# Performance work log

Hardware: AMD Instinct MI355X
Metric: run time of the kernel (lower is better)

## Reference

```python
import jax, jax.numpy as jnp
import numpy as np

K_HALF = 512
BUCKETS = 8
FV_SCALE = 16
SHIFT = 6
FT_SHIFT = 0
FT_IN = 32 * 704 + 704  # FT_IN_DIMS + VIRTUAL = 23232
B = 4096


def setup_inputs() -> dict:
    key = jax.random.key(0)
    ks = jax.random.split(key, 11)
    s = 0.02
    return {
        "bucket": jax.random.randint(ks[0], (B, 1), 0, BUCKETS, dtype=jnp.int64 if jax.config.jax_enable_x64 else jnp.int32).astype(jnp.int32),
        "features1": jax.random.uniform(ks[1], (B, FT_IN), dtype=jnp.float32),
        "features2": jax.random.uniform(ks[2], (B, FT_IN), dtype=jnp.float32),
        "ft_w": s * jax.random.normal(ks[3], (K_HALF + BUCKETS, FT_IN), dtype=jnp.float32),
        "ft_b": s * jax.random.normal(ks[4], (K_HALF + BUCKETS,), dtype=jnp.float32),
        "h1_w": s * jax.random.normal(ks[5], (16 * BUCKETS, 2 * K_HALF), dtype=jnp.float32),
        "h1_b": s * jax.random.normal(ks[6], (16 * BUCKETS,), dtype=jnp.float32),
        "h2_w": s * jax.random.normal(ks[7], (32 * BUCKETS, 16), dtype=jnp.float32),
        "h2_b": s * jax.random.normal(ks[8], (32 * BUCKETS,), dtype=jnp.float32),
        "out_w": s * jax.random.normal(ks[9], (BUCKETS, 32), dtype=jnp.float32),
        "out_b": jnp.zeros((BUCKETS,), dtype=jnp.float32),
    }


def reference(bucket, features1, features2, ft_w, ft_b, h1_w, h1_b, h2_w, h2_b, out_w, out_b):
    clamp = lambda x: jnp.clip(x, 0.0, 1.0)
    a1 = features1 @ ft_w.T + ft_b  # [B, 520]
    a2 = features2 @ ft_w.T + ft_b
    f1, psqt1 = a1[:, :K_HALF], a1[:, K_HALF:]
    f2, psqt2 = a2[:, :K_HALF], a2[:, K_HALF:]
    psqt = 0.5 * (jnp.take_along_axis(psqt1, bucket, axis=1)
                  - jnp.take_along_axis(psqt2, bucket, axis=1))  # [B,1]
    ft_out = clamp(jnp.concatenate([f1, f2], axis=1))  # [B, 1024]
    h1 = (ft_out @ h1_w.T + h1_b).reshape(-1, BUCKETS, 16)
    h1 = clamp(jnp.take_along_axis(h1, bucket[:, :, None], axis=1)[:, 0])  # [B,16]
    h2 = (h1 @ h2_w.T + h2_b).reshape(-1, BUCKETS, 32)
    h2 = clamp(jnp.take_along_axis(h2, bucket[:, :, None], axis=1)[:, 0])  # [B,32]
    out = h2 @ out_w.T + out_b  # [B, 8]
    return jnp.take_along_axis(out, bucket, axis=1) + (FV_SCALE * 2 ** FT_SHIFT) * psqt / 2 ** SHIFT
```

## Files before the change

kernel.cpp:

```cpp
#include <hip/hip_runtime.h>
#include <hip/hip_bf16.h>
#include <stdint.h>

typedef __attribute__((ext_vector_type(8))) short short8v;
typedef __attribute__((ext_vector_type(4))) short short4v;
typedef __attribute__((ext_vector_type(4))) float floatx4;

#define K_DIM   23232
#define BATCH   4096
#define M_TOT   8192
#define BM      128
#define BMG     256
#define BN      176
#define BK      64
#define N_PAD   528
#define N_REAL  520

__device__ __forceinline__ float clamp01(float x) {
    return fminf(fmaxf(x, 0.0f), 1.0f);
}

__device__ __forceinline__ short8v cvt8(float4 a, float4 b) {
    union { short8v s; __hip_bfloat16 h[8]; } u;
    u.h[0] = __float2bfloat16(a.x); u.h[1] = __float2bfloat16(a.y);
    u.h[2] = __float2bfloat16(a.z); u.h[3] = __float2bfloat16(a.w);
    u.h[4] = __float2bfloat16(b.x); u.h[5] = __float2bfloat16(b.y);
    u.h[6] = __float2bfloat16(b.z); u.h[7] = __float2bfloat16(b.w);
    return u.s;
}

#define GLOAD_LDS16(g, l) __builtin_amdgcn_global_load_lds(               \
    (const __attribute__((address_space(1))) void*)(g),                   \
    (__attribute__((address_space(3))) void*)(l), 16, 0, 0)

__global__ __launch_bounds__(256) void convert_bf16(
    const float* __restrict__ f1, const float* __restrict__ f2,
    const float* __restrict__ ftw,
    __hip_bfloat16* __restrict__ A, __hip_bfloat16* __restrict__ B)
{
    const size_t totalA = (size_t)M_TOT * K_DIM;
    const size_t halfA  = totalA / 2;
    const size_t totalB = (size_t)N_PAD * K_DIM;
    const size_t realB  = (size_t)N_REAL * K_DIM;
    size_t idx    = ((size_t)blockIdx.x * blockDim.x + threadIdx.x) * 8;
    size_t stride = (size_t)gridDim.x * blockDim.x * 8;

    for (size_t i = idx; i < totalA; i += stride) {
        const float* src = (i < halfA) ? (f1 + i) : (f2 + (i - halfA));
        float4 v0 = *(const float4*)(src);
        float4 v1 = *(const float4*)(src + 4);
        *(short8v*)(A + i) = cvt8(v0, v1);
    }
    for (size_t i = idx; i < totalB; i += stride) {
        if (i < realB) {
            float4 v0 = *(const float4*)(ftw + i);
            float4 v1 = *(const float4*)(ftw + i + 4);
            *(short8v*)(B + i) = cvt8(v0, v1);
        } else {
            *(short8v*)(B + i) = (short8v){0,0,0,0,0,0,0,0};
        }
    }
}

__global__ __launch_bounds__(256, 2) void ft_gemm(
    const __hip_bfloat16* __restrict__ A,
    const __hip_bfloat16* __restrict__ B,
    float* __restrict__ part, int kiters)
{
    __shared__ __align__(16) __hip_bfloat16 As[BMG][BK];
    __shared__ __align__(16) __hip_bfloat16 Bs[BN][BK];

    const int t    = threadIdx.x;
    const int w    = t >> 6;
    const int lane = t & 63;
    const int quad = lane >> 4;
    const int l16  = lane & 15;
    const int r7   = l16 & 7;

    const int cpx = gridDim.x >> 3;
    const int h   = blockIdx.x;
    const int lid = (h & 7) * cpx + (h >> 3);
    const int xb  = lid % 3;
    const int rst = lid / 3;
    const int yb  = rst & 31;
    const int zb  = rst >> 5;

    const int n0 = xb * BN;
    const int m0 = yb * BMG;
    int k0 = zb * kiters * BK;
    const int kEnd = k0 + kiters * BK;

    const int arow = lane >> 3;
    const int acol = ((lane & 7) ^ (lane >> 3)) * 8;

    floatx4 acc[4][11];
#pragma unroll
    for (int i = 0; i < 4; ++i)
#pragma unroll
        for (int j = 0; j < 11; ++j)
            acc[i][j] = (floatx4){0.f, 0.f, 0.f, 0.f};

    for (; k0 < kEnd; k0 += BK) {
        __syncthreads();
#pragma unroll
        for (int i = 0; i < 8; ++i) {
            int R = w * 8 + i * 32;
            const __hip_bfloat16* g =
                A + (size_t)(m0 + R + arow) * K_DIM + k0 + acol;
            GLOAD_LDS16(g, &As[R][0]);
        }
        for (int R = w * 8; R < BN; R += 32) {
            const __hip_bfloat16* g =
                B + (size_t)(n0 + R + arow) * K_DIM + k0 + acol;
            GLOAD_LDS16(g, &Bs[R][0]);
        }
        __syncthreads();
#pragma unroll
        for (int ks = 0; ks < BK; ks += 32) {
            const int slot = ((ks >> 3) + quad) ^ r7;
            short8v a[4];
#pragma unroll
            for (int mi = 0; mi < 4; ++mi)
                a[mi] = *(const short8v*)(&As[w * 64 + mi * 16 + l16][slot * 8]);
#pragma unroll
            for (int nf = 0; nf < 11; ++nf) {
                short8v b = *(const short8v*)(&Bs[nf * 16 + l16][slot * 8]);
#pragma unroll
                for (int mi = 0; mi < 4; ++mi)
                    acc[mi][nf] = __builtin_amdgcn_mfma_f32_16x16x32_bf16(
                        a[mi], b, acc[mi][nf], 0, 0, 0);
            }
        }
    }

    float* __restrict__ dst = part + (size_t)zb * ((size_t)M_TOT * N_PAD);
#pragma unroll
    for (int mi = 0; mi < 4; ++mi) {
#pragma unroll
        for (int nf = 0; nf < 11; ++nf) {
            int gn = n0 + nf * 16 + l16;
#pragma unroll
            for (int r = 0; r < 4; ++r) {
                int gm = m0 + w * 64 + mi * 16 + quad * 4 + r;
                dst[(size_t)gm * N_PAD + gn] = acc[mi][nf][r];
            }
        }
    }
}

__global__ __launch_bounds__(256) void ft_gemm_fused(
    const float* __restrict__ f1, const float* __restrict__ f2,
    const float* __restrict__ ftw, float* __restrict__ part, int kiters)
{
    __shared__ __align__(16) __hip_bfloat16 As[BM][72];
    __shared__ __align__(16) __hip_bfloat16 Bs[BN][72];

    const int t    = threadIdx.x;
    const int w    = t >> 6;
    const int lane = t & 63;
    const int quad = lane >> 4;
    const int l16  = lane & 15;

    const int n0 = blockIdx.x * BN;
    const int m0 = blockIdx.y * BM;
    const int z  = blockIdx.z;
    int k0 = z * kiters * BK;
    const int kEnd = k0 + kiters * BK;

    const float* __restrict__ srcA =
        (m0 < BATCH) ? (f1 + (size_t)m0 * K_DIM)
                     : (f2 + (size_t)(m0 - BATCH) * K_DIM);

    floatx4 acc[2][11];
#pragma unroll
    for (int i = 0; i < 2; ++i)
#pragma unroll
        for (int j = 0; j < 11; ++j)
            acc[i][j] = (floatx4){0.f, 0.f, 0.f, 0.f};

    for (; k0 < kEnd; k0 += BK) {
        __syncthreads();
#pragma unroll
        for (int it = 0; it < 8; ++it) {
            int c = t + it * 256, row = c >> 4, col = (c & 15) * 4;
            float4 v = *(const float4*)(srcA + (size_t)row * K_DIM + k0 + col);
            union { short4v s; __hip_bfloat16 h[4]; } u;
            u.h[0] = __float2bfloat16(v.x); u.h[1] = __float2bfloat16(v.y);
            u.h[2] = __float2bfloat16(v.z); u.h[3] = __float2bfloat16(v.w);
            *(short4v*)(&As[row][col]) = u.s;
        }
#pragma unroll
        for (int it = 0; it < 11; ++it) {
            int c = t + it * 256, row = c >> 4, col = (c & 15) * 4;
            int gn = n0 + row;
            float4 v = (gn < N_REAL)
                ? *(const float4*)(ftw + (size_t)gn * K_DIM + k0 + col)
                : make_float4(0.f, 0.f, 0.f, 0.f);
            union { short4v s; __hip_bfloat16 h[4]; } u;
            u.h[0] = __float2bfloat16(v.x); u.h[1] = __float2bfloat16(v.y);
            u.h[2] = __float2bfloat16(v.z); u.h[3] = __float2bfloat16(v.w);
            *(short4v*)(&Bs[row][col]) = u.s;
        }
        __syncthreads();
#pragma unroll
        for (int ks = 0; ks < BK; ks += 32) {
            short8v a0 = *(const short8v*)(&As[w * 32 + l16][ks + quad * 8]);
            short8v a1 = *(const short8v*)(&As[w * 32 + 16 + l16][ks + quad * 8]);
#pragma unroll
            for (int nf = 0; nf < 11; ++nf) {
                short8v b = *(const short8v*)(&Bs[nf * 16 + l16][ks + quad * 8]);
                acc[0][nf] = __builtin_amdgcn_mfma_f32_16x16x32_bf16(a0, b, acc[0][nf], 0, 0, 0);
                acc[1][nf] = __builtin_amdgcn_mfma_f32_16x16x32_bf16(a1, b, acc[1][nf], 0, 0, 0);
            }
        }
    }

    float* __restrict__ dst = part + (size_t)z * ((size_t)M_TOT * N_PAD);
#pragma unroll
    for (int mi = 0; mi < 2; ++mi) {
#pragma unroll
        for (int nf = 0; nf < 11; ++nf) {
            int gn = n0 + nf * 16 + l16;
#pragma unroll
            for (int r = 0; r < 4; ++r) {
                int gm = m0 + w * 32 + mi * 16 + quad * 4 + r;
                dst[(size_t)gm * N_PAD + gn] = acc[mi][nf][r];
            }
        }
    }
}

__global__ __launch_bounds__(256) void nnue_tail(
    const float* __restrict__ part, int ksplit,
    const int*   __restrict__ bucket,
    const float* __restrict__ ft_b,
    const float* __restrict__ h1_w, const float* __restrict__ h1_b,
    const float* __restrict__ h2_w, const float* __restrict__ h2_b,
    const float* __restrict__ out_w, const float* __restrict__ out_b,
    float* __restrict__ out)
{
    const int m = blockIdx.x;
    const int b = bucket[m];
    const size_t sz = (size_t)M_TOT * N_PAD;

    __shared__ float ft[1024];
    __shared__ float h1s[16];

    const float* p1 = part + (size_t)m * N_PAD;
    const float* p2 = part + (size_t)(m + BATCH) * N_PAD;

    for (int i = threadIdx.x; i < 1024; i += 256) {
        const float* pr = (i < 512) ? p1 : p2;
        int ci = i & 511;
        float v = ft_b[ci];
        for (int s = 0; s < ksplit; ++s) v += pr[ci + s * sz];
        ft[i] = clamp01(v);
    }
    __syncthreads();

    const int w    = threadIdx.x >> 6;
    const int lane = threadIdx.x & 63;

#pragma unroll
    for (int i = 0; i < 4; ++i) {
        int row = b * 16 + w * 4 + i;
        const float* wr = h1_w + (size_t)row * 1024;
        float s = 0.f;
#pragma unroll
        for (int c = 0; c < 16; ++c)
            s += ft[c * 64 + lane] * wr[c * 64 + lane];
#pragma unroll
        for (int off = 32; off > 0; off >>= 1)
            s += __shfl_down(s, off);
        if (lane == 0) h1s[w * 4 + i] = clamp01(s + h1_b[row]);
    }
    __syncthreads();

    if (threadIdx.x < 32) {
        int i = threadIdx.x;
        const float* wr = h2_w + (size_t)(b * 32 + i) * 16;
        float s = h2_b[b * 32 + i];
#pragma unroll
        for (int j = 0; j < 16; ++j) s += wr[j] * h1s[j];
        float prod = clamp01(s) * out_w[b * 32 + i];
#pragma unroll
        for (int off = 16; off > 0; off >>= 1)
            prod += __shfl_down(prod, off);
        if (i == 0) {
            float v1 = 0.f, v2 = 0.f;
            for (int s2 = 0; s2 < ksplit; ++s2) {
                v1 += p1[512 + b + s2 * sz];
                v2 += p2[512 + b + s2 * sz];
            }
            out[m] = prod + out_b[b] + 0.125f * (v1 - v2);
        }
    }
}

extern "C" void kernel_launch(void* const* d_in, const int* in_sizes, int n_in,
                              void* d_out, int out_size, void* d_ws, size_t ws_size,
                              hipStream_t stream) {
    const int*   bucket = (const int*)  d_in[0];
    const float* f1     = (const float*)d_in[1];
    const float* f2     = (const float*)d_in[2];
    const float* ftw    = (const float*)d_in[3];
    const float* ftb    = (const float*)d_in[4];
    const float* h1w    = (const float*)d_in[5];
    const float* h1b    = (const float*)d_in[6];
    const float* h2w    = (const float*)d_in[7];
    const float* h2b    = (const float*)d_in[8];
    const float* outw   = (const float*)d_in[9];
    const float* outb   = (const float*)d_in[10];
    float* out = (float*)d_out;

    const size_t szA = (size_t)M_TOT * K_DIM * sizeof(__hip_bfloat16);
    const size_t szB = (size_t)N_PAD * K_DIM * sizeof(__hip_bfloat16);
    const size_t szPart1 = (size_t)M_TOT * N_PAD * sizeof(float);

    int ksplit;
    if (ws_size >= szA + szB + 11 * szPart1)      ksplit = 11;
    else if (ws_size >= szA + szB + 3 * szPart1)  ksplit = 3;
    else                                          ksplit = 0;

    if (ksplit > 0) {
        __hip_bfloat16* A = (__hip_bfloat16*)d_ws;
        __hip_bfloat16* Bm = (__hip_bfloat16*)((char*)d_ws + szA);
        float* part = (float*)((char*)d_ws + szA + szB);
        int kiters = 363 / ksplit;

        convert_bf16<<<4096, 256, 0, stream>>>(f1, f2, ftw, A, Bm);
        int nblk = 3 * 32 * ksplit;
        ft_gemm<<<dim3(nblk), 256, 0, stream>>>(A, Bm, part, kiters);
        nnue_tail<<<BATCH, 256, 0, stream>>>(part, ksplit, bucket, ftb,
                                             h1w, h1b, h2w, h2b, outw, outb, out);
    } else {
        float* part = (float*)d_ws;
        dim3 grid1(3, 64, 3);
        ft_gemm_fused<<<grid1, 256, 0, stream>>>(f1, f2, ftw, part, 121);
        nnue_tail<<<BATCH, 256, 0, stream>>>(part, 3, bucket, ftb,
                                             h1w, h1b, h2w, h2b, outw, outb, out);
    }
}
```

Baseline: 1.140 ms.

## Fuse fp32-to-bf16 activation conversion into GEMM A-tile loads

Removes the separate pass that converted both feature matrices to bf16 in workspace. The GEMM now loads fp32 activations directly, converts them in registers and writes them into a swizzled LDS layout, so the large round trip through an intermediate bf16 copy of A is gone. Only the weight matrix is still pre-converted. The tail kernel is also templated on the split count and uses vectorized float4 partial-sum reduction. The trade-off is that A tile loads now go through registers rather than direct global-to-LDS transfers, and each fp32 A element is read once per N tile (three times) at twice the bf16 size.

```diff
diff --git a/kernel.cpp b/kernel.cpp
--- a/kernel.cpp
+++ b/kernel.cpp
@@ -29,28 +29,25 @@
     return u.s;
 }
 
+__device__ __forceinline__ short4v cvt4(float4 a) {
+    union { short4v s; __hip_bfloat16 h[4]; } u;
+    u.h[0] = __float2bfloat16(a.x); u.h[1] = __float2bfloat16(a.y);
+    u.h[2] = __float2bfloat16(a.z); u.h[3] = __float2bfloat16(a.w);
+    return u.s;
+}
+
 #define GLOAD_LDS16(g, l) __builtin_amdgcn_global_load_lds(               \
     (const __attribute__((address_space(1))) void*)(g),                   \
     (__attribute__((address_space(3))) void*)(l), 16, 0, 0)
 
-__global__ __launch_bounds__(256) void convert_bf16(
-    const float* __restrict__ f1, const float* __restrict__ f2,
-    const float* __restrict__ ftw,
-    __hip_bfloat16* __restrict__ A, __hip_bfloat16* __restrict__ B)
+__global__ __launch_bounds__(256) void convert_B(
+    const float* __restrict__ ftw, __hip_bfloat16* __restrict__ B)
 {
-    const size_t totalA = (size_t)M_TOT * K_DIM;
-    const size_t halfA  = totalA / 2;
     const size_t totalB = (size_t)N_PAD * K_DIM;
     const size_t realB  = (size_t)N_REAL * K_DIM;
     size_t idx    = ((size_t)blockIdx.x * blockDim.x + threadIdx.x) * 8;
     size_t stride = (size_t)gridDim.x * blockDim.x * 8;
 
-    for (size_t i = idx; i < totalA; i += stride) {
-        const float* src = (i < halfA) ? (f1 + i) : (f2 + (i - halfA));
-        float4 v0 = *(const float4*)(src);
-        float4 v1 = *(const float4*)(src + 4);
-        *(short8v*)(A + i) = cvt8(v0, v1);
-    }
     for (size_t i = idx; i < totalB; i += stride) {
         if (i < realB) {
             float4 v0 = *(const float4*)(ftw + i);
@@ -62,8 +59,8 @@
     }
 }
 
-__global__ __launch_bounds__(256, 2) void ft_gemm(
-    const __hip_bfloat16* __restrict__ A,
+__global__ __launch_bounds__(256, 2) void ft_gemm_af32(
+    const float* __restrict__ f1, const float* __restrict__ f2,
     const __hip_bfloat16* __restrict__ B,
     float* __restrict__ part, int kiters)
 {
@@ -90,9 +87,19 @@
     int k0 = zb * kiters * BK;
     const int kEnd = k0 + kiters * BK;
 
+    const float* __restrict__ srcA =
+        (m0 < BATCH) ? (f1 + (size_t)m0 * K_DIM)
+                     : (f2 + (size_t)(m0 - BATCH) * K_DIM);
+
     const int arow = lane >> 3;
     const int acol = ((lane & 7) ^ (lane >> 3)) * 8;
 
+    const int tr  = t >> 4;
+    const int c4  = t & 15;
+    const int ps  = (c4 >> 1) ^ (tr & 7);
+    char* const aLds = (char*)&As[0][0] + tr * 128 + ps * 16 + (c4 & 1) * 8;
+    const float* const aG = srcA + (size_t)tr * K_DIM + c4 * 4;
+
     floatx4 acc[4][11];
 #pragma unroll
     for (int i = 0; i < 4; ++i)
@@ -102,17 +109,24 @@
 
     for (; k0 < kEnd; k0 += BK) {
         __syncthreads();
-#pragma unroll
-        for (int i = 0; i < 8; ++i) {
-            int R = w * 8 + i * 32;
-            const __hip_bfloat16* g =
-                A + (size_t)(m0 + R + arow) * K_DIM + k0 + acol;
-            GLOAD_LDS16(g, &As[R][0]);
-        }
         for (int R = w * 8; R < BN; R += 32) {
             const __hip_bfloat16* g =
                 B + (size_t)(n0 + R + arow) * K_DIM + k0 + acol;
             GLOAD_LDS16(g, &Bs[R][0]);
+        }
+        float4 av[4];
+#pragma unroll
+        for (int g4 = 0; g4 < 4; ++g4) {
+#pragma unroll
+            for (int j = 0; j < 4; ++j) {
+                int it = g4 * 4 + j;
+                av[j] = *(const float4*)(aG + (size_t)(it * 16) * K_DIM + k0);
+            }
+#pragma unroll
+            for (int j = 0; j < 4; ++j) {
+                int it = g4 * 4 + j;
+                *(short4v*)(aLds + it * 2048) = cvt4(av[j]);
+            }
         }
         __syncthreads();
 #pragma unroll
@@ -184,10 +198,7 @@
         for (int it = 0; it < 8; ++it) {
             int c = t + it * 256, row = c >> 4, col = (c & 15) * 4;
             float4 v = *(const float4*)(srcA + (size_t)row * K_DIM + k0 + col);
-            union { short4v s; __hip_bfloat16 h[4]; } u;
-            u.h[0] = __float2bfloat16(v.x); u.h[1] = __float2bfloat16(v.y);
-            u.h[2] = __float2bfloat16(v.z); u.h[3] = __float2bfloat16(v.w);
-            *(short4v*)(&As[row][col]) = u.s;
+            *(short4v*)(&As[row][col]) = cvt4(v);
         }
 #pragma unroll
         for (int it = 0; it < 11; ++it) {
@@ -196,10 +207,7 @@
             float4 v = (gn < N_REAL)
                 ? *(const float4*)(ftw + (size_t)gn * K_DIM + k0 + col)
                 : make_float4(0.f, 0.f, 0.f, 0.f);
-            union { short4v s; __hip_bfloat16 h[4]; } u;
-            u.h[0] = __float2bfloat16(v.x); u.h[1] = __float2bfloat16(v.y);
-            u.h[2] = __float2bfloat16(v.z); u.h[3] = __float2bfloat16(v.w);
-            *(short4v*)(&Bs[row][col]) = u.s;
+            *(short4v*)(&Bs[row][col]) = cvt4(v);
         }
         __syncthreads();
 #pragma unroll
@@ -230,8 +238,9 @@
     }
 }
 
-__global__ __launch_bounds__(256) void nnue_tail(
-    const float* __restrict__ part, int ksplit,
+template<int KS>
+__global__ __launch_bounds__(256) void nnue_tail_t(
+    const float* __restrict__ part,
     const int*   __restrict__ bucket,
     const float* __restrict__ ft_b,
     const float* __restrict__ h1_w, const float* __restrict__ h1_b,
@@ -249,12 +258,20 @@
     const float* p1 = part + (size_t)m * N_PAD;
     const float* p2 = part + (size_t)(m + BATCH) * N_PAD;
 
-    for (int i = threadIdx.x; i < 1024; i += 256) {
-        const float* pr = (i < 512) ? p1 : p2;
-        int ci = i & 511;
-        float v = ft_b[ci];
-        for (int s = 0; s < ksplit; ++s) v += pr[ci + s * sz];
-        ft[i] = clamp01(v);
+    {
+        const int t  = threadIdx.x;
+        const float* pr = (t < 128) ? p1 : p2;
+        const int ci = (t & 127) * 4;
+        float4 acc = *(const float4*)(ft_b + ci);
+#pragma unroll
+        for (int s = 0; s < KS; ++s) {
+            float4 v = *(const float4*)(pr + ci + s * sz);
+            acc.x += v.x; acc.y += v.y; acc.z += v.z; acc.w += v.w;
+        }
+        float4 r;
+        r.x = clamp01(acc.x); r.y = clamp01(acc.y);
+        r.z = clamp01(acc.z); r.w = clamp01(acc.w);
+        *(float4*)(ft + t * 4) = r;
     }
     __syncthreads();
 
@@ -288,7 +305,8 @@
             prod += __shfl_down(prod, off);
         if (i == 0) {
             float v1 = 0.f, v2 = 0.f;
-            for (int s2 = 0; s2 < ksplit; ++s2) {
+#pragma unroll
+            for (int s2 = 0; s2 < KS; ++s2) {
                 v1 += p1[512 + b + s2 * sz];
                 v2 += p2[512 + b + s2 * sz];
             }
@@ -313,31 +331,24 @@
     const float* outb   = (const float*)d_in[10];
     float* out = (float*)d_out;
 
-    const size_t szA = (size_t)M_TOT * K_DIM * sizeof(__hip_bfloat16);
     const size_t szB = (size_t)N_PAD * K_DIM * sizeof(__hip_bfloat16);
-    const size_t szPart1 = (size_t)M_TOT * N_PAD * sizeof(float);
-
-    int ksplit;
-    if (ws_size >= szA + szB + 11 * szPart1)      ksplit = 11;
-    else if (ws_size >= szA + szB + 3 * szPart1)  ksplit = 3;
-    else                                          ksplit = 0;
-
-    if (ksplit > 0) {
-        __hip_bfloat16* A = (__hip_bfloat16*)d_ws;
-        __hip_bfloat16* Bm = (__hip_bfloat16*)((char*)d_ws + szA);
-        float* part = (float*)((char*)d_ws + szA + szB);
-        int kiters = 363 / ksplit;
-
-        convert_bf16<<<4096, 256, 0, stream>>>(f1, f2, ftw, A, Bm);
-        int nblk = 3 * 32 * ksplit;
-        ft_gemm<<<dim3(nblk), 256, 0, stream>>>(A, Bm, part, kiters);
-        nnue_tail<<<BATCH, 256, 0, stream>>>(part, ksplit, bucket, ftb,
-                                             h1w, h1b, h2w, h2b, outw, outb, out);
+    const size_t szP = (size_t)M_TOT * N_PAD * sizeof(float);
+
+    if (ws_size >= szB + 11 * szP) {
+        __hip_bfloat16* Bm = (__hip_bfloat16*)d_ws;
+        float* part = (float*)((char*)d_ws + szB);
+
+        convert_B<<<1024, 256, 0, stream>>>(ftw, Bm);
+        ft_gemm_af32<<<dim3(3 * 32 * 11), 256, 0, stream>>>(f1, f2, Bm, part, 33);
+        nnue_tail_t<11><<<BATCH, 256, 0, stream>>>(part, bucket, ftb,
+                                                   h1w, h1b, h2w, h2b,
+                                                   outw, outb, out);
     } else {
         float* part = (float*)d_ws;
         dim3 grid1(3, 64, 3);
         ft_gemm_fused<<<grid1, 256, 0, stream>>>(f1, f2, ftw, part, 121);
-        nnue_tail<<<BATCH, 256, 0, stream>>>(part, 3, bucket, ftb,
-                                             h1w, h1b, h2w, h2b, outw, outb, out);
-    }
-}
+        nnue_tail_t<3><<<BATCH, 256, 0, stream>>>(part, bucket, ftb,
+                                                  h1w, h1b, h2w, h2b,
+                                                  outw, outb, out);
+    }
+}
```

Result: slower. 1.232 ms (+8.1%).
